# Optimization experiments

Measured on AMD Instinct MI355X. Metric: run time of the kernel, lower is better.

Reference implementation:

```python
import jax, jax.numpy as jnp
import numpy as np

# irrep structure for spharms '1x0e+1x1o+1x2e'
DIMS = (1, 3, 5)
OFFS = (0, 1, 4, 9)
N_IRREPS = 3
SPH = 9
MULT = 16          # eq_multiplicity
HEAD = 16          # head_dim
LATENT = 128
ENV_NUMEL = N_IRREPS * MULT            # 48  (MakeWeightedChannels.weight_numel)
LIN_NUMEL = N_IRREPS * MULT * MULT     # 768 (e3nn Linear.weight_numel)
GEN = LATENT + ENV_NUMEL + LIN_NUMEL   # 944 (generate_n_weights)
N = 8192
E = 65536
ISQRTD = 4         # math.isqrt(HEAD); source MULTIPLIES scores by this
EPS = 1e-5


def setup_inputs() -> dict:
    key = jax.random.key(0)
    ks = jax.random.split(key, 12)
    h = jax.random.normal(ks[0], (N, LATENT), jnp.float32)
    X = jax.random.normal(ks[1], (N, MULT, SPH), jnp.float32)
    t_ij = jax.random.normal(ks[2], (E, LATENT), jnp.float32)
    spharms = jax.random.normal(ks[3], (E, SPH), jnp.float32)
    phi_ij = jax.random.normal(ks[4], (E, 8), jnp.float32)  # unused by forward (as in source)
    edge_center = jax.random.randint(ks[5], (E,), 0, N)
    edge_neighbor = jax.random.randint(ks[6], (E,), 0, N)
    s = 1.0 / np.sqrt(LATENT).astype(np.float32)
    W_rs = jax.random.normal(ks[7], (LATENT, GEN), jnp.float32) * s
    W1 = jax.random.normal(ks[8], (LATENT, LATENT), jnp.float32) * s   # h_j_emb MLP layer 1
    W2 = jax.random.normal(ks[9], (LATENT, GEN), jnp.float32) * s      # h_j_emb MLP layer 2
    ln_gamma = jnp.ones((LATENT,), jnp.float32)
    ln_beta = jnp.zeros((LATENT,), jnp.float32)
    W_query = jax.random.normal(ks[10], (LATENT, MULT * HEAD), jnp.float32) * s
    W_key = jax.random.normal(ks[11], (LATENT, MULT * HEAD), jnp.float32) * s
    return dict(h=h, X=X, t_ij=t_ij, spharms=spharms, phi_ij=phi_ij,
                edge_center=edge_center, edge_neighbor=edge_neighbor,
                W_rs=W_rs, W1=W1, W2=W2, ln_gamma=ln_gamma, ln_beta=ln_beta,
                W_query=W_query, W_key=W_key, num_nodes=N)


def _layernorm(x, g, b):
    mu = jnp.mean(x, -1, keepdims=True)
    var = jnp.var(x, -1, keepdims=True)
    return (x - mu) * jax.lax.rsqrt(var + EPS) * g + b


def _so3_layernorm(x):
    # per-node, per-irrep RMS normalization over (mult, components); equivariant
    outs = []
    for i in range(N_IRREPS):
        blk = x[..., OFFS[i]:OFFS[i + 1]]
        rms = jnp.sqrt(jnp.mean(blk * blk, axis=(-2, -1), keepdims=True) + EPS)
        outs.append(blk / rms)
    return jnp.concatenate(outs, -1)


def _env_weighter(sph, w):
    # MakeWeightedChannels: per-edge weight [E, n_irreps, mult] broadcast over irrep components
    w = w.reshape(-1, N_IRREPS, MULT)
    w_exp = jnp.repeat(w, np.array(DIMS), axis=1)        # [E, SPH, MULT]
    return jnp.einsum('es,esm->ems', sph, w_exp)          # [E, MULT, SPH]


def _eq_linear(x, w):
    # e3nn Linear with external per-edge weights: per-irrep [mult,mult] mixing, 1/sqrt(fan_in)
    w = w.reshape(-1, N_IRREPS, MULT, MULT) / np.sqrt(MULT).astype(np.float32)
    outs = [jnp.einsum('euv,evd->eud', w[:, i], x[..., OFFS[i]:OFFS[i + 1]])
            for i in range(N_IRREPS)]
    return jnp.concatenate(outs, -1)


def _scatter_softmax(logits, seg, n):
    m = jax.ops.segment_max(logits, seg, num_segments=n)
    m = jnp.where(jnp.isfinite(m), m, 0.0)
    ex = jnp.exp(logits - m[seg])
    den = jax.ops.segment_sum(ex, seg, num_segments=n)
    return ex / (den[seg] + 1e-20)


def reference(h, X, t_ij, spharms, phi_ij, edge_center, edge_neighbor,
              W_rs, W1, W2, ln_gamma, ln_beta, W_query, W_key, num_nodes):
    h_j = h[edge_neighbor]                                   # [E, D] edge gather
    env_ij_scalar = t_ij @ W_rs                              # [E, GEN]
    env_j_scalar = jax.nn.silu(h_j @ W1) @ W2                # h_j_emb MLP, [E, GEN]
    env_ij_w = env_ij_scalar * env_j_scalar
    # scalar update
    delta_h = jax.ops.segment_sum(env_ij_w[:, :LATENT], edge_center, num_segments=num_nodes)
    h_new = _layernorm(h + delta_h, ln_gamma, ln_beta)
    # generated weights (NB: source bug -- env slice overlaps latent slice; replicated)
    env_w = env_ij_w[:, :ENV_NUMEL]
    lin_w = env_ij_w[:, ENV_NUMEL:ENV_NUMEL + LIN_NUMEL]
    delta_spharm = _env_weighter(spharms, env_w)             # [E, MULT, SPH]
    delta_eq = _eq_linear(X[edge_neighbor], lin_w)           # [E, MULT, SPH]
    x = delta_spharm + delta_eq
    # attention with scatter-softmax grouped by edge_center
    Q = (t_ij @ W_query).reshape(-1, MULT, HEAD)
    K = (h_j @ W_key).reshape(-1, MULT, HEAD)
    scores = jnp.einsum('emh,emh->em', Q, K) * ISQRTD
    alpha = _scatter_softmax(scores, edge_center, num_nodes)  # [E, MULT]
    delta_X = jax.ops.segment_sum(x * alpha[:, :, None], edge_center, num_segments=num_nodes)
    X_new = _so3_layernorm(X + delta_X)
    return h_new, X_new, t_ij
```

## Files before the change

kernel.cpp:

```cpp
#include <hip/hip_runtime.h>

#define N_NODES 8192
#define N_EDGES 65536
#define LAT 128
#define GEN 944
#define ECOLS 816
#define ENVN 48
#define LINN 768
#define MULT 16
#define SPH 9
#define XROW 144

#define EM 16
#define NWT 51
#define WTCOLS 816
#define WPAD 824

#define SB 64
#define KC 16

#define OFF_WT    ((size_t)0)
#define OFF_ENV   ((size_t)52224)
#define OFF_KN    (OFF_ENV  + (size_t)N_NODES*ECOLS)
#define OFF_EX    (OFF_KN   + (size_t)N_NODES*256)
#define OFF_DH    (OFF_EX   + (size_t)N_EDGES*MULT)
#define OFF_DX    (OFF_DH   + (size_t)N_NODES*LAT)
#define OFF_DEN   (OFF_DX   + (size_t)N_NODES*XROW)
#define OFF_NMAX  (OFF_DEN  + (size_t)N_NODES*MULT)
#define OFF_XBUF  (OFF_NMAX + (size_t)N_NODES*MULT)

typedef __attribute__((ext_vector_type(8))) short bf16x8;
typedef __attribute__((ext_vector_type(4))) float f32x4;

__device__ __forceinline__ unsigned fkey(float f) {
  unsigned u = __float_as_uint(f);
  return (u & 0x80000000u) ? ~u : (u | 0x80000000u);
}
__device__ __forceinline__ float fdecode(unsigned u) {
  u = (u & 0x80000000u) ? (u & 0x7fffffffu) : ~u;
  return __uint_as_float(u);
}
__device__ __forceinline__ ushort f2b(float f) {
  unsigned u = __float_as_uint(f);
  return (ushort)((u + 0x7FFFu + ((u >> 16) & 1u)) >> 16);
}
__device__ __forceinline__ float b2f(ushort u) {
  return __uint_as_float(((unsigned)u) << 16);
}

__global__ __launch_bounds__(128) void k_wt(
    const float* __restrict__ W_rs, ushort* __restrict__ Wt) {
  int c = blockIdx.x;
  int k = threadIdx.x;
  Wt[(size_t)c * 128 + k] = f2b(W_rs[(size_t)k * GEN + c]);
}

__global__ __launch_bounds__(256) void k_node(
    const float* __restrict__ h, const float* __restrict__ W1,
    const float* __restrict__ W2, const float* __restrict__ Wk,
    float* __restrict__ env_node, float* __restrict__ Knode) {
  __shared__ float h_lds[8][LAT];
  __shared__ float s_lds[8][LAT];
  const int tid = threadIdx.x;
  const int nb = blockIdx.x * 8;

  { int o = tid * 4, e = o >> 7, k = o & 127;
    *(float4*)&h_lds[e][k] = *(const float4*)&h[(size_t)(nb + e) * LAT + k]; }
  __syncthreads();

  {
    int e = tid >> 5, c4 = (tid & 31) * 4;
    float a0 = 0, a1 = 0, a2 = 0, a3 = 0;
    for (int k0 = 0; k0 < LAT; k0 += 4) {
      float4 tv = *(float4*)&h_lds[e][k0];
      float4 w0 = *(const float4*)&W1[(k0 + 0) * LAT + c4];
      float4 w1 = *(const float4*)&W1[(k0 + 1) * LAT + c4];
      float4 w2 = *(const float4*)&W1[(k0 + 2) * LAT + c4];
      float4 w3 = *(const float4*)&W1[(k0 + 3) * LAT + c4];
      a0 += tv.x * w0.x + tv.y * w1.x + tv.z * w2.x + tv.w * w3.x;
      a1 += tv.x * w0.y + tv.y * w1.y + tv.z * w2.y + tv.w * w3.y;
      a2 += tv.x * w0.z + tv.y * w1.z + tv.z * w2.z + tv.w * w3.z;
      a3 += tv.x * w0.w + tv.y * w1.w + tv.z * w2.w + tv.w * w3.w;
    }
    s_lds[e][c4 + 0] = a0 / (1.f + expf(-a0));
    s_lds[e][c4 + 1] = a1 / (1.f + expf(-a1));
    s_lds[e][c4 + 2] = a2 / (1.f + expf(-a2));
    s_lds[e][c4 + 3] = a3 / (1.f + expf(-a3));
  }
  {
    int e = tid >> 5;
#pragma unroll
    for (int t2 = 0; t2 < 2; ++t2) {
      int c4 = ((tid & 31) + 32 * t2) * 4;
      float a0 = 0, a1 = 0, a2 = 0, a3 = 0;
      for (int k0 = 0; k0 < LAT; k0 += 4) {
        float4 tv = *(float4*)&h_lds[e][k0];
        float4 w0 = *(const float4*)&Wk[(k0 + 0) * 256 + c4];
        float4 w1 = *(const float4*)&Wk[(k0 + 1) * 256 + c4];
        float4 w2 = *(const float4*)&Wk[(k0 + 2) * 256 + c4];
        float4 w3 = *(const float4*)&Wk[(k0 + 3) * 256 + c4];
        a0 += tv.x * w0.x + tv.y * w1.x + tv.z * w2.x + tv.w * w3.x;
        a1 += tv.x * w0.y + tv.y * w1.y + tv.z * w2.y + tv.w * w3.y;
        a2 += tv.x * w0.z + tv.y * w1.z + tv.z * w2.z + tv.w * w3.z;
        a3 += tv.x * w0.w + tv.y * w1.w + tv.z * w2.w + tv.w * w3.w;
      }
      float4 r = make_float4(a0, a1, a2, a3);
      *(float4*)&Knode[(size_t)(nb + e) * 256 + c4] = r;
    }
  }
  __syncthreads();

  if (tid < 204) {
    int c4 = tid * 4;
    float4 acc[8];
#pragma unroll
    for (int e = 0; e < 8; ++e) acc[e] = make_float4(0, 0, 0, 0);
    for (int k0 = 0; k0 < LAT; k0 += 4) {
      float4 w0 = *(const float4*)&W2[(size_t)(k0 + 0) * GEN + c4];
      float4 w1 = *(const float4*)&W2[(size_t)(k0 + 1) * GEN + c4];
      float4 w2 = *(const float4*)&W2[(size_t)(k0 + 2) * GEN + c4];
      float4 w3 = *(const float4*)&W2[(size_t)(k0 + 3) * GEN + c4];
#pragma unroll
      for (int e = 0; e < 8; ++e) {
        float4 tv = *(float4*)&s_lds[e][k0];
        acc[e].x += tv.x * w0.x + tv.y * w1.x + tv.z * w2.x + tv.w * w3.x;
        acc[e].y += tv.x * w0.y + tv.y * w1.y + tv.z * w2.y + tv.w * w3.y;
        acc[e].z += tv.x * w0.z + tv.y * w1.z + tv.z * w2.z + tv.w * w3.z;
        acc[e].w += tv.x * w0.w + tv.y * w1.w + tv.z * w2.w + tv.w * w3.w;
      }
    }
#pragma unroll
    for (int e = 0; e < 8; ++e)
      *(float4*)&env_node[(size_t)(nb + e) * ECOLS + c4] = acc[e];
  }
}

__global__ __launch_bounds__(256) void k_edge(
    const float* __restrict__ t_ij, const float* __restrict__ X,
    const float* __restrict__ sph, const int* __restrict__ ectr,
    const int* __restrict__ enbr, const ushort* __restrict__ Wt,
    const float* __restrict__ env_node, float* __restrict__ delta_h,
    ushort* __restrict__ x_buf) {
  __shared__ ushort w_lds[EM][WPAD];
  __shared__ float xj_lds[EM][SPH][16];
  __shared__ float sph_lds[EM][12];
  __shared__ int i_lds[EM], j_lds[EM];
  const int tid = threadIdx.x;
  const int lane = tid & 63;
  const int wid = tid >> 6;
  const int eb = blockIdx.x * EM;
  const int r15 = lane & 15, kg = lane >> 4;

  if (tid < EM) { i_lds[tid] = ectr[eb + tid]; j_lds[tid] = enbr[eb + tid]; }
  if (tid < EM * SPH) {
    int e = tid / 9, s = tid % 9;
    sph_lds[e][s] = sph[(size_t)(eb + e) * SPH + s];
  }
  for (int o = tid; o < EM * XROW; o += 256) {
    int e = o / XROW, rr = o % XROW, v = rr / 9, s = rr % 9;
    xj_lds[e][s][v] = X[(size_t)enbr[eb + e] * XROW + rr];
  }

  bf16x8 ahi[4], alo[4];
#pragma unroll
  for (int c = 0; c < 4; ++c) {
    const float* src = &t_ij[(size_t)(eb + r15) * LAT + c * 32 + kg * 8];
    float f[8];
    *(float4*)&f[0] = *(const float4*)src;
    *(float4*)&f[4] = *(const float4*)(src + 4);
    bf16x8 hh, ll;
#pragma unroll
    for (int d = 0; d < 8; ++d) {
      ushort hb = f2b(f[d]);
      hh[d] = hb;
      ll[d] = f2b(f[d] - b2f(hb));
    }
    ahi[c] = hh; alo[c] = ll;
  }
  __syncthreads();

  for (int tn = wid; tn < NWT; tn += 4) {
    const ushort* b0 = &Wt[(size_t)(tn * 16 + r15) * 128 + kg * 8];
    f32x4 acc = {0.f, 0.f, 0.f, 0.f};
#pragma unroll
    for (int c = 0; c < 4; ++c) {
      bf16x8 b = *(const bf16x8*)(b0 + c * 32);
      acc = __builtin_amdgcn_mfma_f32_16x16x32_bf16(ahi[c], b, acc, 0, 0, 0);
      acc = __builtin_amdgcn_mfma_f32_16x16x32_bf16(alo[c], b, acc, 0, 0, 0);
    }
    int col = tn * 16 + r15;
#pragma unroll
    for (int g = 0; g < 4; ++g) {
      int row = kg * 4 + g;
      int j = j_lds[row];
      float v = acc[g] * env_node[(size_t)j * ECOLS + col];
      w_lds[row][col] = f2b(v);
      if (tn < 8)
        atomicAdd(&delta_h[(size_t)i_lds[row] * LAT + col], v);
    }
  }
  __syncthreads();

  {
    int e = tid >> 4, m = tid & 15;
    float lw[3][16], ew[3];
#pragma unroll
    for (int ir = 0; ir < 3; ++ir) {
      const ushort* p = &w_lds[e][ENVN + ir * 256 + m * 16];
      uint4 q0 = *(const uint4*)p;
      uint4 q1 = *(const uint4*)(p + 8);
      unsigned qq[8] = {q0.x, q0.y, q0.z, q0.w, q1.x, q1.y, q1.z, q1.w};
#pragma unroll
      for (int d = 0; d < 8; ++d) {
        lw[ir][2 * d]     = __uint_as_float(qq[d] << 16);
        lw[ir][2 * d + 1] = __uint_as_float(qq[d] & 0xFFFF0000u);
      }
      ew[ir] = b2f(w_lds[e][ir * 16 + m]);
    }
    ushort* xp = &x_buf[((size_t)(eb + e) * MULT + m) * SPH];
#pragma unroll
    for (int s = 0; s < SPH; ++s) {
      int ir = (s == 0) ? 0 : ((s < 4) ? 1 : 2);
      const float* xr = xj_lds[e][s];
      float acc = sph_lds[e][s] * ew[ir];
#pragma unroll
      for (int v4 = 0; v4 < 4; ++v4) {
        float4 xv = *(const float4*)&xr[v4 * 4];
        acc += 0.25f * (lw[ir][v4 * 4 + 0] * xv.x + lw[ir][v4 * 4 + 1] * xv.y +
                        lw[ir][v4 * 4 + 2] * xv.z + lw[ir][v4 * 4 + 3] * xv.w);
      }
      xp[s] = f2b(acc);
    }
  }
}

__global__ __launch_bounds__(256) void k_score(
    const float* __restrict__ t_ij, const int* __restrict__ ectr,
    const int* __restrict__ enbr, const float* __restrict__ Wq,
    const float* __restrict__ Knode, float* __restrict__ ex_buf,
    unsigned* __restrict__ nmax) {
  __shared__ float t_lds[SB][129];
  __shared__ float wq_lds[KC][260];
  const int tid = threadIdx.x;
  const int eb = blockIdx.x * SB;
  const int m = tid & 15, eg = tid >> 4;
  const int rot = (m >> 1) & 3;

#pragma unroll
  for (int p = 0; p < 8; ++p) {
    int qi = tid + p * 256;
    int e = qi >> 5, kq = (qi & 31) * 4;
    float4 v = *(const float4*)&t_ij[(size_t)(eb + e) * LAT + kq];
    t_lds[e][kq + 0] = v.x; t_lds[e][kq + 1] = v.y;
    t_lds[e][kq + 2] = v.z; t_lds[e][kq + 3] = v.w;
  }

  float qa[4][16];
#pragma unroll
  for (int e = 0; e < 4; ++e)
#pragma unroll
    for (int hh = 0; hh < 16; ++hh) qa[e][hh] = 0.f;

  for (int kc = 0; kc < LAT; kc += KC) {
    __syncthreads();
#pragma unroll
    for (int p = 0; p < 4; ++p) {
      int idx = tid + p * 256;
      int kr = idx >> 6, c4 = (idx & 63) * 4;
      int mm = c4 >> 4, h4 = (c4 >> 2) & 3;
      int c4s = mm * 16 + ((h4 + (mm >> 1)) & 3) * 4;
      float4 v = *(const float4*)&Wq[(size_t)(kc + kr) * 256 + c4];
      *(float4*)&wq_lds[kr][c4s] = v;
    }
    __syncthreads();
#pragma unroll 2
    for (int kk = 0; kk < KC; ++kk) {
      float w[16];
#pragma unroll
      for (int i = 0; i < 4; ++i) {
        float4 wv = *(const float4*)&wq_lds[kk][m * 16 + ((i + rot) & 3) * 4];
        w[i * 4 + 0] = wv.x; w[i * 4 + 1] = wv.y;
        w[i * 4 + 2] = wv.z; w[i * 4 + 3] = wv.w;
      }
#pragma unroll
      for (int e = 0; e < 4; ++e) {
        float tv = t_lds[eg * 4 + e][kc + kk];
#pragma unroll
        for (int hh = 0; hh < 16; ++hh) qa[e][hh] += tv * w[hh];
      }
    }
  }

#pragma unroll
  for (int e = 0; e < 4; ++e) {
    int ee = eb + eg * 4 + e;
    int j = enbr[ee];
    const float* kn = &Knode[(size_t)j * 256 + m * 16];
    float4 k0 = *(const float4*)kn;
    float4 k1 = *(const float4*)(kn + 4);
    float4 k2 = *(const float4*)(kn + 8);
    float4 k3 = *(const float4*)(kn + 12);
    float acc =
        qa[e][0] * k0.x + qa[e][1] * k0.y + qa[e][2] * k0.z + qa[e][3] * k0.w +
        qa[e][4] * k1.x + qa[e][5] * k1.y + qa[e][6] * k1.z + qa[e][7] * k1.w +
        qa[e][8] * k2.x + qa[e][9] * k2.y + qa[e][10] * k2.z + qa[e][11] * k2.w +
        qa[e][12] * k3.x + qa[e][13] * k3.y + qa[e][14] * k3.z + qa[e][15] * k3.w;
    float sc = 4.f * acc;
    ex_buf[(size_t)ee * MULT + m] = sc;
    atomicMax(&nmax[ectr[ee] * MULT + m], fkey(sc));
  }
}

__global__ __launch_bounds__(256) void k_den(
    const int* __restrict__ ectr, const unsigned* __restrict__ nmax,
    float* __restrict__ ex_buf, float* __restrict__ den) {
  int idx = blockIdx.x * 256 + threadIdx.x;
  int e = idx >> 4, m = idx & 15;
  int i = ectr[e];
  float mval = fdecode(nmax[i * MULT + m]);
  float ex = expf(ex_buf[idx] - mval);
  ex_buf[idx] = ex;
  atomicAdd(&den[i * MULT + m], ex);
}

__global__ __launch_bounds__(256) void k_dx(
    const int* __restrict__ ectr, const float* __restrict__ ex_buf,
    const float* __restrict__ den, const ushort* __restrict__ x_buf,
    float* __restrict__ delta_X) {
  size_t idx = (size_t)blockIdx.x * 256 + threadIdx.x;
  int e = (int)(idx / XROW), r = (int)(idx % XROW), m = r / SPH;
  int i = ectr[e];
  float alpha = ex_buf[(size_t)e * MULT + m] / (den[i * MULT + m] + 1e-20f);
  atomicAdd(&delta_X[(size_t)i * XROW + r], b2f(x_buf[idx]) * alpha);
}

__global__ __launch_bounds__(64) void k_hout(
    const float* __restrict__ h, const float* __restrict__ dh,
    const float* __restrict__ gamma, const float* __restrict__ beta,
    float* __restrict__ out) {
  int n = blockIdx.x, lane = threadIdx.x;
  size_t base = (size_t)n * LAT + lane * 2;
  float2 hv = *(const float2*)&h[base];
  float2 dv = *(const float2*)&dh[base];
  float v0 = hv.x + dv.x, v1 = hv.y + dv.y;
  float s = v0 + v1, ss = v0 * v0 + v1 * v1;
#pragma unroll
  for (int o = 32; o; o >>= 1) { s += __shfl_xor(s, o); ss += __shfl_xor(ss, o); }
  float mean = s * (1.f / 128.f);
  float var = ss * (1.f / 128.f) - mean * mean;
  float inv = rsqrtf(var + 1e-5f);
  int c = lane * 2;
  out[base + 0] = (v0 - mean) * inv * gamma[c + 0] + beta[c + 0];
  out[base + 1] = (v1 - mean) * inv * gamma[c + 1] + beta[c + 1];
}

__global__ __launch_bounds__(192) void k_xout(
    const float* __restrict__ X, const float* __restrict__ dX,
    float* __restrict__ out) {
  __shared__ float ssq[3];
  int n = blockIdx.x, tid = threadIdx.x;
  if (tid < 3) ssq[tid] = 0.f;
  __syncthreads();
  float val = 0.f; int ir = 0;
  if (tid < XROW) {
    val = X[(size_t)n * XROW + tid] + dX[(size_t)n * XROW + tid];
    int s = tid % SPH;
    ir = (s == 0) ? 0 : ((s < 4) ? 1 : 2);
    atomicAdd(&ssq[ir], val * val);
  }
  __syncthreads();
  if (tid < XROW) {
    const float cnt[3] = {16.f, 48.f, 80.f};
    float rms = sqrtf(ssq[ir] / cnt[ir] + 1e-5f);
    out[(size_t)n * XROW + tid] = val / rms;
  }
}

extern "C" void kernel_launch(void* const* d_in, const int* in_sizes, int n_in,
                              void* d_out, int out_size, void* d_ws, size_t ws_size,
                              hipStream_t stream) {
  const float* h    = (const float*)d_in[0];
  const float* X    = (const float*)d_in[1];
  const float* t_ij = (const float*)d_in[2];
  const float* sph  = (const float*)d_in[3];
  const int*   ectr = (const int*)d_in[5];
  const int*   enbr = (const int*)d_in[6];
  const float* W_rs = (const float*)d_in[7];
  const float* W1   = (const float*)d_in[8];
  const float* W2   = (const float*)d_in[9];
  const float* gam  = (const float*)d_in[10];
  const float* bet  = (const float*)d_in[11];
  const float* Wq   = (const float*)d_in[12];
  const float* Wk   = (const float*)d_in[13];
  float* out = (float*)d_out;
  float* ws  = (float*)d_ws;

  ushort*   Wt       = (ushort*)(ws + OFF_WT);
  float*    env_node = ws + OFF_ENV;
  float*    Knode    = ws + OFF_KN;
  float*    ex_buf   = ws + OFF_EX;
  float*    delta_h  = ws + OFF_DH;
  float*    delta_X  = ws + OFF_DX;
  float*    den      = ws + OFF_DEN;
  unsigned* nmax     = (unsigned*)(ws + OFF_NMAX);
  ushort*   x_buf    = (ushort*)(ws + OFF_XBUF);

  hipMemsetAsync(delta_h, 0,
                 (size_t)N_NODES * (LAT + XROW + MULT + MULT) * sizeof(float), stream);
  hipMemcpyAsync(out + (size_t)N_NODES * (LAT + XROW), d_in[2],
                 (size_t)N_EDGES * LAT * sizeof(float),
                 hipMemcpyDeviceToDevice, stream);

  k_wt<<<WTCOLS, 128, 0, stream>>>(W_rs, Wt);
  k_node<<<N_NODES / 8, 256, 0, stream>>>(h, W1, W2, Wk, env_node, Knode);
  k_edge<<<N_EDGES / EM, 256, 0, stream>>>(t_ij, X, sph, ectr, enbr, Wt,
                                           env_node, delta_h, x_buf);
  k_score<<<N_EDGES / SB, 256, 0, stream>>>(t_ij, ectr, enbr, Wq, Knode,
                                            ex_buf, nmax);
  k_den<<<(N_EDGES * MULT) / 256, 256, 0, stream>>>(ectr, nmax, ex_buf, den);
  k_dx<<<((size_t)N_EDGES * XROW) / 256, 256, 0, stream>>>(ectr, ex_buf, den, x_buf, delta_X);
  k_hout<<<N_NODES, 64, 0, stream>>>(h, delta_h, gam, bet, out);
  k_xout<<<N_NODES, 192, 0, stream>>>(X, delta_X, out + (size_t)N_NODES * LAT);
}
```

Measured before the change: 594.6 us.

## Store node env weights and gathered X in bf16, prefetch next weight tile

Stores the per-node env_node matrix as bf16 instead of fp32, which halves the gather traffic for the random neighbor lookups in the edge kernel. Neighbor X rows are kept in LDS as bf16. The MFMA loop is software-pipelined so the next tile's Wt fragment and env_node values are loaded while the current tile is computed. Row offsets are also hoisted out of the loop. The cost is extra rounding in env weights and X, plus higher register pressure from the double-buffered operands.

```diff
diff --git a/kernel.cpp b/kernel.cpp
--- a/kernel.cpp
+++ b/kernel.cpp
@@ -21,7 +21,7 @@
 
 #define OFF_WT    ((size_t)0)
 #define OFF_ENV   ((size_t)52224)
-#define OFF_KN    (OFF_ENV  + (size_t)N_NODES*ECOLS)
+#define OFF_KN    (OFF_ENV  + (size_t)N_NODES*ECOLS/2)
 #define OFF_EX    (OFF_KN   + (size_t)N_NODES*256)
 #define OFF_DH    (OFF_EX   + (size_t)N_EDGES*MULT)
 #define OFF_DX    (OFF_DH   + (size_t)N_NODES*LAT)
@@ -58,7 +58,7 @@
 __global__ __launch_bounds__(256) void k_node(
     const float* __restrict__ h, const float* __restrict__ W1,
     const float* __restrict__ W2, const float* __restrict__ Wk,
-    float* __restrict__ env_node, float* __restrict__ Knode) {
+    ushort* __restrict__ env_node, float* __restrict__ Knode) {
   __shared__ float h_lds[8][LAT];
   __shared__ float s_lds[8][LAT];
   const int tid = threadIdx.x;
@@ -130,8 +130,12 @@
       }
     }
 #pragma unroll
-    for (int e = 0; e < 8; ++e)
-      *(float4*)&env_node[(size_t)(nb + e) * ECOLS + c4] = acc[e];
+    for (int e = 0; e < 8; ++e) {
+      ushort4 r;
+      r.x = f2b(acc[e].x); r.y = f2b(acc[e].y);
+      r.z = f2b(acc[e].z); r.w = f2b(acc[e].w);
+      *(ushort4*)&env_node[(size_t)(nb + e) * ECOLS + c4] = r;
+    }
   }
 }
 
@@ -139,17 +143,17 @@
     const float* __restrict__ t_ij, const float* __restrict__ X,
     const float* __restrict__ sph, const int* __restrict__ ectr,
     const int* __restrict__ enbr, const ushort* __restrict__ Wt,
-    const float* __restrict__ env_node, float* __restrict__ delta_h,
+    const ushort* __restrict__ env_node, float* __restrict__ delta_h,
     ushort* __restrict__ x_buf) {
   __shared__ ushort w_lds[EM][WPAD];
-  __shared__ float xj_lds[EM][SPH][16];
+  __shared__ ushort xj_lds[EM][SPH][16];
   __shared__ float sph_lds[EM][12];
   __shared__ int i_lds[EM], j_lds[EM];
   const int tid = threadIdx.x;
   const int lane = tid & 63;
   const int wid = tid >> 6;
   const int eb = blockIdx.x * EM;
-  const int r15 = lane & 15, kg = lane >> 4;
+  const int r15 = lane & 15, kg = lane >> 4, kg4 = kg * 4;
 
   if (tid < EM) { i_lds[tid] = ectr[eb + tid]; j_lds[tid] = enbr[eb + tid]; }
   if (tid < EM * SPH) {
@@ -158,7 +162,7 @@
   }
   for (int o = tid; o < EM * XROW; o += 256) {
     int e = o / XROW, rr = o % XROW, v = rr / 9, s = rr % 9;
-    xj_lds[e][s][v] = X[(size_t)enbr[eb + e] * XROW + rr];
+    xj_lds[e][s][v] = f2b(X[(size_t)enbr[eb + e] * XROW + rr]);
   }
 
   bf16x8 ahi[4], alo[4];
@@ -179,24 +183,52 @@
   }
   __syncthreads();
 
+  int jrow[4], irow[4];
+#pragma unroll
+  for (int g = 0; g < 4; ++g) {
+    jrow[g] = j_lds[kg4 + g] * ECOLS;
+    irow[g] = i_lds[kg4 + g] * LAT;
+  }
+
+  bf16x8 bA[4]; ushort eA[4];
+  {
+    const ushort* b0 = &Wt[(size_t)(wid * 16 + r15) * 128 + kg * 8];
+#pragma unroll
+    for (int c = 0; c < 4; ++c) bA[c] = *(const bf16x8*)(b0 + c * 32);
+    int col = wid * 16 + r15;
+#pragma unroll
+    for (int g = 0; g < 4; ++g) eA[g] = env_node[(size_t)jrow[g] + col];
+  }
   for (int tn = wid; tn < NWT; tn += 4) {
-    const ushort* b0 = &Wt[(size_t)(tn * 16 + r15) * 128 + kg * 8];
+    const int tn2 = tn + 4;
+    bf16x8 bB[4]; ushort eB[4];
+    if (tn2 < NWT) {
+      const ushort* b0 = &Wt[(size_t)(tn2 * 16 + r15) * 128 + kg * 8];
+#pragma unroll
+      for (int c = 0; c < 4; ++c) bB[c] = *(const bf16x8*)(b0 + c * 32);
+      int col2 = tn2 * 16 + r15;
+#pragma unroll
+      for (int g = 0; g < 4; ++g) eB[g] = env_node[(size_t)jrow[g] + col2];
+    }
     f32x4 acc = {0.f, 0.f, 0.f, 0.f};
 #pragma unroll
     for (int c = 0; c < 4; ++c) {
-      bf16x8 b = *(const bf16x8*)(b0 + c * 32);
-      acc = __builtin_amdgcn_mfma_f32_16x16x32_bf16(ahi[c], b, acc, 0, 0, 0);
-      acc = __builtin_amdgcn_mfma_f32_16x16x32_bf16(alo[c], b, acc, 0, 0, 0);
+      acc = __builtin_amdgcn_mfma_f32_16x16x32_bf16(ahi[c], bA[c], acc, 0, 0, 0);
+      acc = __builtin_amdgcn_mfma_f32_16x16x32_bf16(alo[c], bA[c], acc, 0, 0, 0);
     }
     int col = tn * 16 + r15;
 #pragma unroll
     for (int g = 0; g < 4; ++g) {
-      int row = kg * 4 + g;
-      int j = j_lds[row];
-      float v = acc[g] * env_node[(size_t)j * ECOLS + col];
-      w_lds[row][col] = f2b(v);
+      float v = acc[g] * b2f(eA[g]);
+      w_lds[kg4 + g][col] = f2b(v);
       if (tn < 8)
-        atomicAdd(&delta_h[(size_t)i_lds[row] * LAT + col], v);
+        atomicAdd(&delta_h[(size_t)irow[g] + col], v);
+    }
+    if (tn2 < NWT) {
+#pragma unroll
+      for (int c = 0; c < 4; ++c) bA[c] = bB[c];
+#pragma unroll
+      for (int g = 0; g < 4; ++g) eA[g] = eB[g];
     }
   }
   __syncthreads();
@@ -221,13 +253,16 @@
 #pragma unroll
     for (int s = 0; s < SPH; ++s) {
       int ir = (s == 0) ? 0 : ((s < 4) ? 1 : 2);
-      const float* xr = xj_lds[e][s];
+      const ushort* xr = xj_lds[e][s];
+      uint4 x0 = *(const uint4*)xr;
+      uint4 x1 = *(const uint4*)(xr + 8);
+      unsigned xx[8] = {x0.x, x0.y, x0.z, x0.w, x1.x, x1.y, x1.z, x1.w};
       float acc = sph_lds[e][s] * ew[ir];
 #pragma unroll
-      for (int v4 = 0; v4 < 4; ++v4) {
-        float4 xv = *(const float4*)&xr[v4 * 4];
-        acc += 0.25f * (lw[ir][v4 * 4 + 0] * xv.x + lw[ir][v4 * 4 + 1] * xv.y +
-                        lw[ir][v4 * 4 + 2] * xv.z + lw[ir][v4 * 4 + 3] * xv.w);
+      for (int d = 0; d < 8; ++d) {
+        float v0 = __uint_as_float(xx[d] << 16);
+        float v1 = __uint_as_float(xx[d] & 0xFFFF0000u);
+        acc += 0.25f * (lw[ir][2 * d] * v0 + lw[ir][2 * d + 1] * v1);
       }
       xp[s] = f2b(acc);
     }
@@ -396,7 +431,7 @@
   float* ws  = (float*)d_ws;
 
   ushort*   Wt       = (ushort*)(ws + OFF_WT);
-  float*    env_node = ws + OFF_ENV;
+  ushort*   env_node = (ushort*)(ws + OFF_ENV);
   float*    Knode    = ws + OFF_KN;
   float*    ex_buf   = ws + OFF_EX;
   float*    delta_h  = ws + OFF_DH;
```

Result: faster. 479.2 us (-19.4%).
